# Kernel optimization log

Measured on AMD Instinct MI355X. Metric: run time of the kernel, lower is better.

## Reference

```python
import jax, jax.numpy as jnp
import numpy as np

D = 1024
H = 16
HD = D // H
EPS = 1e-8


def setup_inputs() -> dict:
    key = jax.random.key(0)
    ks = jax.random.split(key, 12)
    B, S = 2, 2048
    scale = 1.0 / np.sqrt(D)
    inp = {
        "x": jax.random.normal(ks[0], (B, S, D), dtype=jnp.float32),
        "M": jax.random.uniform(ks[1], (B, S, S), dtype=jnp.float32),
        "Wq": jax.random.normal(ks[2], (D, D), dtype=jnp.float32) * scale,
        "bq": jax.random.normal(ks[3], (D,), dtype=jnp.float32) * 0.01,
        "Wk": jax.random.normal(ks[4], (D, D), dtype=jnp.float32) * scale,
        "bk": jax.random.normal(ks[5], (D,), dtype=jnp.float32) * 0.01,
        "Wv": jax.random.normal(ks[6], (D, D), dtype=jnp.float32) * scale,
        "bv": jax.random.normal(ks[7], (D,), dtype=jnp.float32) * 0.01,
        "Wo": jax.random.normal(ks[8], (D, D), dtype=jnp.float32) * scale,
        "bo": jax.random.normal(ks[9], (D,), dtype=jnp.float32) * 0.01,
    }
    return inp


def reference(x, M, Wq, bq, Wk, bk, Wv, bv, Wo, bo):
    B, S, _ = x.shape
    sm_scale = HD ** -0.5
    # projections (torch Linear: x @ W^T + b), split into heads: [B,H,S,HD]
    def proj(W, b):
        return (x @ W.T + b).reshape(B, S, H, HD).transpose(0, 2, 1, 3)
    Q, K, V = proj(Wq, bq), proj(Wk, bk), proj(Wv, bv)
    # scores: [B,H,S,S], gated pre-softmax by M broadcast over heads
    scores = jnp.einsum("bhqd,bhkd->bhqk", Q, K) * sm_scale
    Mb = M[:, None, :, :]  # [B,1,S,S]
    scores = scores * Mb
    attn = jax.nn.softmax(scores, axis=-1)
    # post-softmax re-gate + L1 renormalize
    A_sparse = attn * Mb
    norm = jnp.sum(jnp.abs(A_sparse), axis=-1, keepdims=True) + EPS
    A_bar = A_sparse / norm
    out = jnp.einsum("bhqk,bhkd->bhqd", A_bar, V)
    out = out.transpose(0, 2, 1, 3).reshape(B, S, D)
    return out @ Wo.T + bo
```

## Files before the change

kernel.cpp:

```cpp
#include <hip/hip_runtime.h>
#include <hip/hip_bf16.h>
#include <stdint.h>

#define S_LEN 2048
#define D_DIM 1024
#define NROW 4096
#define EPS_F 1e-8f

typedef __attribute__((ext_vector_type(8))) short short8;
typedef __attribute__((ext_vector_type(4))) float f32x4;

__device__ __forceinline__ unsigned short f2bf(float f) {
  uint32_t u = __float_as_uint(f);
  u += 0x7fffu + ((u >> 16) & 1u);
  return (unsigned short)(u >> 16);
}

__global__ void convert_kernel(const float* __restrict__ x,
                               const float* __restrict__ wq, const float* __restrict__ wk,
                               const float* __restrict__ wv, const float* __restrict__ wo,
                               unsigned short* __restrict__ xb, unsigned short* __restrict__ wqb,
                               unsigned short* __restrict__ wkb, unsigned short* __restrict__ wvb,
                               unsigned short* __restrict__ wob) {
  const float* src; unsigned short* dst; int n;
  switch (blockIdx.y) {
    case 0: src = x;  dst = xb;  n = NROW * D_DIM;  break;
    case 1: src = wq; dst = wqb; n = D_DIM * D_DIM; break;
    case 2: src = wk; dst = wkb; n = D_DIM * D_DIM; break;
    case 3: src = wv; dst = wvb; n = D_DIM * D_DIM; break;
    default: src = wo; dst = wob; n = D_DIM * D_DIM; break;
  }
  int idx = blockIdx.x * blockDim.x + threadIdx.x;
  int base = idx * 8;
  if (base >= n) return;
  f32x4 va = *(const f32x4*)(src + base);
  f32x4 vb = *(const f32x4*)(src + base + 4);
  short8 o;
  o[0] = (short)f2bf(va[0]); o[1] = (short)f2bf(va[1]);
  o[2] = (short)f2bf(va[2]); o[3] = (short)f2bf(va[3]);
  o[4] = (short)f2bf(vb[0]); o[5] = (short)f2bf(vb[1]);
  o[6] = (short)f2bf(vb[2]); o[7] = (short)f2bf(vb[3]);
  *(short8*)(dst + base) = o;
}

template<int MODE>
__global__ __launch_bounds__(256) void gemm_bt(const unsigned short* __restrict__ A,
                                               const unsigned short* __restrict__ Bw,
                                               const float* __restrict__ bias,
                                               void* __restrict__ Cout, float scale) {
  __shared__ unsigned short As[128 * 72];
  __shared__ unsigned short Bs[128 * 72];
  const int t = threadIdx.x;
  const int lane = t & 63;
  const int w = t >> 6;
  const int wm = w >> 1, wn = w & 1;
  const int m0 = blockIdx.x * 128, n0 = blockIdx.y * 128;
  const int g = lane >> 4, c0 = lane & 15;

  f32x4 acc[4][4] = {};
  short8 ra[4], rb[4];

#define G_LOADT(kt) { int kk = (kt) * 64; \
    _Pragma("unroll") for (int i = 0; i < 4; ++i) { int c = i * 256 + t; int row = c >> 3, c8 = c & 7; \
      ra[i] = *(const short8*)(A  + (size_t)(m0 + row) * D_DIM + kk + c8 * 8); \
      rb[i] = *(const short8*)(Bw + (size_t)(n0 + row) * D_DIM + kk + c8 * 8); } }
#define G_WRITET() { \
    _Pragma("unroll") for (int i = 0; i < 4; ++i) { int c = i * 256 + t; int row = c >> 3, c8 = c & 7; \
      *(short8*)&As[row * 72 + c8 * 8] = ra[i]; \
      *(short8*)&Bs[row * 72 + c8 * 8] = rb[i]; } }

  G_LOADT(0); G_WRITET(); __syncthreads();

  for (int kt = 0; kt < 16; ++kt) {
    if (kt < 15) G_LOADT(kt + 1);
#pragma unroll
    for (int kc = 0; kc < 2; ++kc) {
      short8 af[4], bf[4];
#pragma unroll
      for (int mf = 0; mf < 4; ++mf)
        af[mf] = *(const short8*)&As[(wm * 64 + mf * 16 + c0) * 72 + kc * 32 + g * 8];
#pragma unroll
      for (int nf = 0; nf < 4; ++nf)
        bf[nf] = *(const short8*)&Bs[(wn * 64 + nf * 16 + c0) * 72 + kc * 32 + g * 8];
#pragma unroll
      for (int mf = 0; mf < 4; ++mf)
#pragma unroll
        for (int nf = 0; nf < 4; ++nf)
          acc[mf][nf] = __builtin_amdgcn_mfma_f32_16x16x32_bf16(af[mf], bf[nf], acc[mf][nf], 0, 0, 0);
    }
    __syncthreads();
    if (kt < 15) { G_WRITET(); __syncthreads(); }
  }

#pragma unroll
  for (int nf = 0; nf < 4; ++nf) {
    int jj = n0 + wn * 64 + nf * 16 + c0;
    float bval = bias[jj];
#pragma unroll
    for (int mf = 0; mf < 4; ++mf) {
#pragma unroll
      for (int r = 0; r < 4; ++r) {
        int ii = m0 + wm * 64 + mf * 16 + g * 4 + r;
        float v = (acc[mf][nf][r] + bval) * scale;
        if (MODE == 2) {
          ((float*)Cout)[(size_t)ii * D_DIM + jj] = v;
        } else if (MODE == 0) {
          size_t addr = ((size_t)((ii >> 11) * 16 + (jj >> 6)) * 2048 + (ii & 2047)) * 64 + (jj & 63);
          ((unsigned short*)Cout)[addr] = f2bf(v);
        } else {
          size_t addr = ((size_t)(ii >> 11) * 1024 + jj) * 2048 + (ii & 2047);
          ((unsigned short*)Cout)[addr] = f2bf(v);
        }
      }
    }
  }
#undef G_LOADT
#undef G_WRITET
}

__global__ __launch_bounds__(512, 4) void attn_kernel(const unsigned short* __restrict__ Qg,
                                                      const unsigned short* __restrict__ Kg,
                                                      const unsigned short* __restrict__ Vtg,
                                                      const float* __restrict__ Mg,
                                                      unsigned short* __restrict__ aout) {
  __shared__ unsigned short Ks[2][64 * 72];
  __shared__ unsigned short Vts[2][64 * 72];
  __shared__ unsigned short Ps[128 * 72];

  const int t = threadIdx.x;
  const int lane = t & 63;
  const int w = t >> 6;
  const int g = lane >> 4, c0 = lane & 15;
  const int bh = blockIdx.x;
  const int q0 = blockIdx.y * 128;
  const int b = bh >> 4;

  const unsigned short* Qbase  = Qg  + ((size_t)bh * 2048 + q0) * 64;
  const unsigned short* Kbase  = Kg  + (size_t)bh * 2048 * 64;
  const unsigned short* Vtbase = Vtg + (size_t)bh * 64 * 2048;
  const float* Mlane = Mg + ((size_t)b * 2048 + q0 + w * 16 + g * 4) * 2048 + c0;

  short8 qf[2];
#pragma unroll
  for (int kc = 0; kc < 2; ++kc)
    qf[kc] = *(const short8*)(Qbase + (size_t)(w * 16 + c0) * 64 + kc * 32 + g * 8);

  f32x4 o[4] = {};
  float dpe[4] = {0.f, 0.f, 0.f, 0.f};
  float de[4]  = {0.f, 0.f, 0.f, 0.f};

  short8 rk, rv;
  const int srow = t >> 3, sc8 = t & 7;

#define A_LOAD(kt) { int k0 = (kt) * 64; \
    rk = *(const short8*)(Kbase  + (size_t)(k0 + srow) * 64 + sc8 * 8); \
    rv = *(const short8*)(Vtbase + (size_t)srow * 2048 + k0 + sc8 * 8); }
#define A_WRITE(bufi) { \
    *(short8*)&Ks[bufi][srow * 72 + sc8 * 8]  = rk; \
    *(short8*)&Vts[bufi][srow * 72 + sc8 * 8] = rv; }

  A_LOAD(0); A_WRITE(0); __syncthreads();

  for (int kt = 0; kt < 32; ++kt) {
    const int cur = kt & 1;
    if (kt < 31) A_LOAD(kt + 1);

    float mv[4][4];
    {
      const float* Mk = Mlane + kt * 64;
#pragma unroll
      for (int nf = 0; nf < 4; ++nf)
#pragma unroll
        for (int r = 0; r < 4; ++r)
          mv[nf][r] = Mk[(size_t)r * 2048 + nf * 16];
    }

    f32x4 sf[4] = {};
#pragma unroll
    for (int kc = 0; kc < 2; ++kc) {
      short8 kf[4];
#pragma unroll
      for (int nf = 0; nf < 4; ++nf)
        kf[nf] = *(const short8*)&Ks[cur][(nf * 16 + c0) * 72 + kc * 32 + g * 8];
#pragma unroll
      for (int nf = 0; nf < 4; ++nf)
        sf[nf] = __builtin_amdgcn_mfma_f32_16x16x32_bf16(qf[kc], kf[nf], sf[nf], 0, 0, 0);
    }

#pragma unroll
    for (int nf = 0; nf < 4; ++nf)
#pragma unroll
      for (int r = 0; r < 4; ++r) {
        float m = mv[nf][r];
        float e  = __expf(sf[nf][r] * m);
        float pe = m * e;
        dpe[r] += pe;
        de[r]  += e;
        uint32_t u = __float_as_uint(pe) + 0x8000u;
        Ps[(w * 16 + g * 4 + r) * 72 + nf * 16 + c0] = (unsigned short)(u >> 16);
      }

    asm volatile("s_waitcnt lgkmcnt(0)" ::: "memory");
    __builtin_amdgcn_sched_barrier(0);

#pragma unroll
    for (int kc = 0; kc < 2; ++kc) {
      short8 pf = *(const short8*)&Ps[(w * 16 + c0) * 72 + kc * 32 + g * 8];
#pragma unroll
      for (int df = 0; df < 4; ++df) {
        short8 vf = *(const short8*)&Vts[cur][(df * 16 + c0) * 72 + kc * 32 + g * 8];
        o[df] = __builtin_amdgcn_mfma_f32_16x16x32_bf16(pf, vf, o[df], 0, 0, 0);
      }
    }

    if (kt < 31) A_WRITE(cur ^ 1);
    __syncthreads();
  }

#pragma unroll
  for (int xm = 1; xm <= 8; xm <<= 1)
#pragma unroll
    for (int r = 0; r < 4; ++r) {
      dpe[r] += __shfl_xor(dpe[r], xm);
      de[r]  += __shfl_xor(de[r], xm);
    }
  float inv[4];
#pragma unroll
  for (int r = 0; r < 4; ++r)
    inv[r] = 1.0f / (dpe[r] + EPS_F * de[r]);

#pragma unroll
  for (int df = 0; df < 4; ++df)
#pragma unroll
    for (int r = 0; r < 4; ++r) {
      float v = o[df][r] * inv[r];
      int qi = q0 + w * 16 + g * 4 + r;
      int col = (bh & 15) * 64 + df * 16 + c0;
      aout[((size_t)b * 2048 + qi) * 1024 + col] = f2bf(v);
    }
#undef A_LOAD
#undef A_WRITE
}

extern "C" void kernel_launch(void* const* d_in, const int* in_sizes, int n_in,
                              void* d_out, int out_size, void* d_ws, size_t ws_size,
                              hipStream_t stream) {
  const float* x  = (const float*)d_in[0];
  const float* M  = (const float*)d_in[1];
  const float* Wq = (const float*)d_in[2];
  const float* bq = (const float*)d_in[3];
  const float* Wk = (const float*)d_in[4];
  const float* bk = (const float*)d_in[5];
  const float* Wv = (const float*)d_in[6];
  const float* bv = (const float*)d_in[7];
  const float* Wo = (const float*)d_in[8];
  const float* bo = (const float*)d_in[9];
  float* out = (float*)d_out;
  char* ws = (char*)d_ws;

  unsigned short* xb   = (unsigned short*)(ws);
  unsigned short* wqb  = (unsigned short*)(ws + 8388608);
  unsigned short* wkb  = (unsigned short*)(ws + 10485760);
  unsigned short* wvb  = (unsigned short*)(ws + 12582912);
  unsigned short* wob  = (unsigned short*)(ws + 14680064);
  unsigned short* Qb   = (unsigned short*)(ws + 16777216);
  unsigned short* Kb   = (unsigned short*)(ws + 25165824);
  unsigned short* Vtb  = (unsigned short*)(ws + 33554432);
  unsigned short* aoutb= (unsigned short*)(ws + 41943040);

  convert_kernel<<<dim3(2048, 5), 256, 0, stream>>>(x, Wq, Wk, Wv, Wo, xb, wqb, wkb, wvb, wob);
  gemm_bt<0><<<dim3(32, 8), 256, 0, stream>>>(xb, wqb, bq, (void*)Qb, 0.125f);
  gemm_bt<0><<<dim3(32, 8), 256, 0, stream>>>(xb, wkb, bk, (void*)Kb, 1.0f);
  gemm_bt<1><<<dim3(32, 8), 256, 0, stream>>>(xb, wvb, bv, (void*)Vtb, 1.0f);
  attn_kernel<<<dim3(32, 16), 512, 0, stream>>>(Qb, Kb, Vtb, M, aoutb);
  gemm_bt<2><<<dim3(32, 8), 256, 0, stream>>>(aoutb, wob, bo, (void*)out, 1.0f);
}
```

Before: 166.8 us.

## Fuse QKV GEMM, pre-layout mask in fp16, register-resident P in attention

Fuses the three QKV projections into a single GEMM over a concatenated weight matrix, and switches GEMM tile loads to direct global-to-LDS loads without padding. A new pass converts the mask M to fp16 in the MFMA fragment order so attention reads half the bytes with vectorized loads. The attention kernel swaps MFMA operand order so P stays in registers, exchanged across lanes with ds_bpermute instead of an LDS round trip. It also drops the eps*sum(e) term from the normalizer and packs the output with v_cvt_pk_bf16_f32. Risks include bank conflicts in the unpadded LDS, a synchronous GEMM load loop with no prefetch, an extra pass over M, and small numerical differences from the fp16 mask and the removed eps term.

```diff
diff --git a/kernel.cpp b/kernel.cpp
--- a/kernel.cpp
+++ b/kernel.cpp
@@ -5,33 +5,41 @@
 #define S_LEN 2048
 #define D_DIM 1024
 #define NROW 4096
-#define EPS_F 1e-8f
 
 typedef __attribute__((ext_vector_type(8))) short short8;
 typedef __attribute__((ext_vector_type(4))) float f32x4;
-
-__device__ __forceinline__ unsigned short f2bf(float f) {
+typedef __attribute__((ext_vector_type(4))) int i32x4;
+typedef __attribute__((ext_vector_type(8))) _Float16 h8;
+typedef unsigned short ushort_t;
+
+__device__ __forceinline__ ushort_t f2bf(float f) {
   uint32_t u = __float_as_uint(f);
   u += 0x7fffu + ((u >> 16) & 1u);
-  return (unsigned short)(u >> 16);
-}
-
-__global__ void convert_kernel(const float* __restrict__ x,
-                               const float* __restrict__ wq, const float* __restrict__ wk,
-                               const float* __restrict__ wv, const float* __restrict__ wo,
-                               unsigned short* __restrict__ xb, unsigned short* __restrict__ wqb,
-                               unsigned short* __restrict__ wkb, unsigned short* __restrict__ wvb,
-                               unsigned short* __restrict__ wob) {
-  const float* src; unsigned short* dst; int n;
+  return (ushort_t)(u >> 16);
+}
+
+__device__ __forceinline__ ushort_t f2h(float f) {
+  _Float16 h = (_Float16)f;
+  return __builtin_bit_cast(ushort_t, h);
+}
+
+__device__ __forceinline__ void gload16(const void* g, void* l) {
+  __builtin_amdgcn_global_load_lds((const __attribute__((address_space(1))) void*)g,
+                                   (__attribute__((address_space(3))) void*)l, 16, 0, 0);
+}
+
+__global__ void convert4_kernel(const float* __restrict__ x,
+                                const float* __restrict__ wq, const float* __restrict__ wk,
+                                const float* __restrict__ wv,
+                                ushort_t* __restrict__ xb, ushort_t* __restrict__ wcat) {
+  const float* src; ushort_t* dst; int n;
   switch (blockIdx.y) {
-    case 0: src = x;  dst = xb;  n = NROW * D_DIM;  break;
-    case 1: src = wq; dst = wqb; n = D_DIM * D_DIM; break;
-    case 2: src = wk; dst = wkb; n = D_DIM * D_DIM; break;
-    case 3: src = wv; dst = wvb; n = D_DIM * D_DIM; break;
-    default: src = wo; dst = wob; n = D_DIM * D_DIM; break;
-  }
-  int idx = blockIdx.x * blockDim.x + threadIdx.x;
-  int base = idx * 8;
+    case 0: src = x;  dst = xb;             n = NROW * D_DIM;  break;
+    case 1: src = wq; dst = wcat;           n = D_DIM * D_DIM; break;
+    case 2: src = wk; dst = wcat + 1048576; n = D_DIM * D_DIM; break;
+    default: src = wv; dst = wcat + 2097152; n = D_DIM * D_DIM; break;
+  }
+  int base = (blockIdx.x * 256 + threadIdx.x) * 8;
   if (base >= n) return;
   f32x4 va = *(const f32x4*)(src + base);
   f32x4 vb = *(const f32x4*)(src + base + 4);
@@ -43,45 +51,74 @@
   *(short8*)(dst + base) = o;
 }
 
+__global__ void convert_wo_kernel(const float* __restrict__ wo, ushort_t* __restrict__ wob) {
+  int base = (blockIdx.x * 256 + threadIdx.x) * 8;
+  f32x4 va = *(const f32x4*)(wo + base);
+  f32x4 vb = *(const f32x4*)(wo + base + 4);
+  short8 o;
+  o[0] = (short)f2bf(va[0]); o[1] = (short)f2bf(va[1]);
+  o[2] = (short)f2bf(va[2]); o[3] = (short)f2bf(va[3]);
+  o[4] = (short)f2bf(vb[0]); o[5] = (short)f2bf(vb[1]);
+  o[6] = (short)f2bf(vb[2]); o[7] = (short)f2bf(vb[3]);
+  *(short8*)(wob + base) = o;
+}
+
+__global__ __launch_bounds__(256) void m2_transform(const float* __restrict__ M,
+                                                    ushort_t* __restrict__ M2) {
+  int tid = blockIdx.x * 256 + threadIdx.x;
+  int lane = tid & 63, w = (tid >> 6) & 7, kt = (tid >> 9) & 31, combo = tid >> 14;
+  int c0 = lane & 15, g = lane >> 4;
+  int b = combo >> 4, q0i = combo & 15;
+  const float* src = M + ((size_t)b * 2048 + q0i * 128 + w * 16 + c0) * 2048 + kt * 64 + g * 4;
+  ushort_t outv[16];
+#pragma unroll
+  for (int nf = 0; nf < 4; ++nf) {
+    f32x4 v = *(const f32x4*)(src + nf * 16);
+#pragma unroll
+    for (int r = 0; r < 4; ++r)
+      outv[nf * 4 + r] = f2h(v[r]);
+  }
+  *(short8*)(M2 + (size_t)tid * 16)     = *(short8*)&outv[0];
+  *(short8*)(M2 + (size_t)tid * 16 + 8) = *(short8*)&outv[8];
+}
+
 template<int MODE>
-__global__ __launch_bounds__(256) void gemm_bt(const unsigned short* __restrict__ A,
-                                               const unsigned short* __restrict__ Bw,
-                                               const float* __restrict__ bias,
-                                               void* __restrict__ Cout, float scale) {
-  __shared__ unsigned short As[128 * 72];
-  __shared__ unsigned short Bs[128 * 72];
+__global__ __launch_bounds__(256, 4) void gemm_glds(const ushort_t* __restrict__ A,
+                                                    const ushort_t* __restrict__ Bw,
+                                                    const float* __restrict__ bias0,
+                                                    const float* __restrict__ bias1,
+                                                    const float* __restrict__ bias2,
+                                                    void* __restrict__ Cout) {
+  __shared__ ushort_t As[128 * 64];
+  __shared__ ushort_t Bs[128 * 64];
   const int t = threadIdx.x;
   const int lane = t & 63;
   const int w = t >> 6;
   const int wm = w >> 1, wn = w & 1;
   const int m0 = blockIdx.x * 128, n0 = blockIdx.y * 128;
   const int g = lane >> 4, c0 = lane & 15;
+  const int srow = lane >> 3, scol = (lane & 7) * 8;
 
   f32x4 acc[4][4] = {};
-  short8 ra[4], rb[4];
-
-#define G_LOADT(kt) { int kk = (kt) * 64; \
-    _Pragma("unroll") for (int i = 0; i < 4; ++i) { int c = i * 256 + t; int row = c >> 3, c8 = c & 7; \
-      ra[i] = *(const short8*)(A  + (size_t)(m0 + row) * D_DIM + kk + c8 * 8); \
-      rb[i] = *(const short8*)(Bw + (size_t)(n0 + row) * D_DIM + kk + c8 * 8); } }
-#define G_WRITET() { \
-    _Pragma("unroll") for (int i = 0; i < 4; ++i) { int c = i * 256 + t; int row = c >> 3, c8 = c & 7; \
-      *(short8*)&As[row * 72 + c8 * 8] = ra[i]; \
-      *(short8*)&Bs[row * 72 + c8 * 8] = rb[i]; } }
-
-  G_LOADT(0); G_WRITET(); __syncthreads();
 
   for (int kt = 0; kt < 16; ++kt) {
-    if (kt < 15) G_LOADT(kt + 1);
+    const int kk = kt * 64;
+#pragma unroll
+    for (int i = 0; i < 4; ++i) {
+      gload16(A  + (size_t)(m0 + w * 32 + i * 8 + srow) * D_DIM + kk + scol, &As[(w * 32 + i * 8) * 64]);
+      gload16(Bw + (size_t)(n0 + w * 32 + i * 8 + srow) * D_DIM + kk + scol, &Bs[(w * 32 + i * 8) * 64]);
+    }
+    asm volatile("s_waitcnt vmcnt(0)" ::: "memory");
+    __syncthreads();
 #pragma unroll
     for (int kc = 0; kc < 2; ++kc) {
       short8 af[4], bf[4];
 #pragma unroll
       for (int mf = 0; mf < 4; ++mf)
-        af[mf] = *(const short8*)&As[(wm * 64 + mf * 16 + c0) * 72 + kc * 32 + g * 8];
+        af[mf] = *(const short8*)&As[(wm * 64 + mf * 16 + c0) * 64 + kc * 32 + g * 8];
 #pragma unroll
       for (int nf = 0; nf < 4; ++nf)
-        bf[nf] = *(const short8*)&Bs[(wn * 64 + nf * 16 + c0) * 72 + kc * 32 + g * 8];
+        bf[nf] = *(const short8*)&Bs[(wn * 64 + nf * 16 + c0) * 64 + kc * 32 + g * 8];
 #pragma unroll
       for (int mf = 0; mf < 4; ++mf)
 #pragma unroll
@@ -89,56 +126,64 @@
           acc[mf][nf] = __builtin_amdgcn_mfma_f32_16x16x32_bf16(af[mf], bf[nf], acc[mf][nf], 0, 0, 0);
     }
     __syncthreads();
-    if (kt < 15) { G_WRITET(); __syncthreads(); }
   }
 
 #pragma unroll
   for (int nf = 0; nf < 4; ++nf) {
     int jj = n0 + wn * 64 + nf * 16 + c0;
-    float bval = bias[jj];
+    float bval;
+    if (MODE == 0) {
+      int proj = jj >> 10, jcol = jj & 1023;
+      const float* bp = (proj == 0) ? bias0 : ((proj == 1) ? bias1 : bias2);
+      bval = bp[jcol];
+    } else {
+      bval = bias0[jj];
+    }
 #pragma unroll
     for (int mf = 0; mf < 4; ++mf) {
 #pragma unroll
       for (int r = 0; r < 4; ++r) {
         int ii = m0 + wm * 64 + mf * 16 + g * 4 + r;
-        float v = (acc[mf][nf][r] + bval) * scale;
+        float v = acc[mf][nf][r] + bval;
         if (MODE == 2) {
           ((float*)Cout)[(size_t)ii * D_DIM + jj] = v;
-        } else if (MODE == 0) {
-          size_t addr = ((size_t)((ii >> 11) * 16 + (jj >> 6)) * 2048 + (ii & 2047)) * 64 + (jj & 63);
-          ((unsigned short*)Cout)[addr] = f2bf(v);
         } else {
-          size_t addr = ((size_t)(ii >> 11) * 1024 + jj) * 2048 + (ii & 2047);
-          ((unsigned short*)Cout)[addr] = f2bf(v);
+          int proj = jj >> 10, jcol = jj & 1023;
+          if (proj == 0) v *= 0.125f;
+          int bb = ii >> 11, s = ii & 2047;
+          size_t addr;
+          if (proj < 2) {
+            int hcol = jcol >> 6, hd = jcol & 63;
+            addr = (size_t)proj * 4194304 + ((size_t)(bb * 16 + hcol) * 2048 + s) * 64 + hd;
+          } else {
+            addr = (size_t)2 * 4194304 + ((size_t)bb * 1024 + jcol) * 2048 + s;
+          }
+          ((ushort_t*)Cout)[addr] = f2bf(v);
         }
       }
     }
   }
-#undef G_LOADT
-#undef G_WRITET
-}
-
-__global__ __launch_bounds__(512, 4) void attn_kernel(const unsigned short* __restrict__ Qg,
-                                                      const unsigned short* __restrict__ Kg,
-                                                      const unsigned short* __restrict__ Vtg,
-                                                      const float* __restrict__ Mg,
-                                                      unsigned short* __restrict__ aout) {
-  __shared__ unsigned short Ks[2][64 * 72];
-  __shared__ unsigned short Vts[2][64 * 72];
-  __shared__ unsigned short Ps[128 * 72];
-
-  const int t = threadIdx.x;
-  const int lane = t & 63;
-  const int w = t >> 6;
+}
+
+__global__ __launch_bounds__(512, 4) void attn_kernel(const ushort_t* __restrict__ Qg,
+                                                      const ushort_t* __restrict__ Kg,
+                                                      const ushort_t* __restrict__ Vtg,
+                                                      const ushort_t* __restrict__ M2,
+                                                      ushort_t* __restrict__ aout) {
+  __shared__ ushort_t Ks[2][64 * 72];
+  __shared__ ushort_t Vts[2][64 * 72];
+
+  const int t = threadIdx.x, lane = t & 63, w = t >> 6;
   const int g = lane >> 4, c0 = lane & 15;
-  const int bh = blockIdx.x;
-  const int q0 = blockIdx.y * 128;
-  const int b = bh >> 4;
-
-  const unsigned short* Qbase  = Qg  + ((size_t)bh * 2048 + q0) * 64;
-  const unsigned short* Kbase  = Kg  + (size_t)bh * 2048 * 64;
-  const unsigned short* Vtbase = Vtg + (size_t)bh * 64 * 2048;
-  const float* Mlane = Mg + ((size_t)b * 2048 + q0 + w * 16 + g * 4) * 2048 + c0;
+  const int id = blockIdx.x;
+  const int r8 = id & 7, hh = (id >> 3) & 15, ss = id >> 7;
+  const int combo = r8 + 8 * ss, b = combo >> 4, q0 = (combo & 15) * 128;
+  const int bh = b * 16 + hh;
+
+  const ushort_t* Qbase  = Qg  + ((size_t)bh * 2048 + q0) * 64;
+  const ushort_t* Kbase  = Kg  + (size_t)bh * 2048 * 64;
+  const ushort_t* Vtbase = Vtg + (size_t)bh * 64 * 2048;
+  const ushort_t* M2base = M2 + ((size_t)combo * 32 * 8 + w) * 64 * 16 + (size_t)lane * 16;
 
   short8 qf[2];
 #pragma unroll
@@ -146,33 +191,31 @@
     qf[kc] = *(const short8*)(Qbase + (size_t)(w * 16 + c0) * 64 + kc * 32 + g * 8);
 
   f32x4 o[4] = {};
-  float dpe[4] = {0.f, 0.f, 0.f, 0.f};
-  float de[4]  = {0.f, 0.f, 0.f, 0.f};
-
-  short8 rk, rv;
-  const int srow = t >> 3, sc8 = t & 7;
-
-#define A_LOAD(kt) { int k0 = (kt) * 64; \
-    rk = *(const short8*)(Kbase  + (size_t)(k0 + srow) * 64 + sc8 * 8); \
-    rv = *(const short8*)(Vtbase + (size_t)srow * 2048 + k0 + sc8 * 8); }
-#define A_WRITE(bufi) { \
-    *(short8*)&Ks[bufi][srow * 72 + sc8 * 8]  = rk; \
-    *(short8*)&Vts[bufi][srow * 72 + sc8 * 8] = rv; }
-
-  A_LOAD(0); A_WRITE(0); __syncthreads();
+  float dpe = 0.f;
+  const int idxA = (((g & 1) * 2 + (g >> 1)) * 16 + c0) * 4;
+  const int idxB = (((g & 1) * 2 + 1 - (g >> 1)) * 16 + c0) * 4;
+  const bool glo = (g < 2);
+  const bool gb = (g & 1);
+
+  const int srow = t >> 3, sc8 = (t & 7) * 8;
+  short8 rk, rv, rm0, rm1, rm0n, rm1n;
+
+  rk  = *(const short8*)(Kbase + (size_t)srow * 64 + sc8);
+  rv  = *(const short8*)(Vtbase + (size_t)srow * 2048 + sc8);
+  rm0 = *(const short8*)(M2base);
+  rm1 = *(const short8*)(M2base + 8);
+  *(short8*)&Ks[0][srow * 72 + sc8]  = rk;
+  *(short8*)&Vts[0][srow * 72 + sc8] = rv;
+  __syncthreads();
 
   for (int kt = 0; kt < 32; ++kt) {
     const int cur = kt & 1;
-    if (kt < 31) A_LOAD(kt + 1);
-
-    float mv[4][4];
-    {
-      const float* Mk = Mlane + kt * 64;
-#pragma unroll
-      for (int nf = 0; nf < 4; ++nf)
-#pragma unroll
-        for (int r = 0; r < 4; ++r)
-          mv[nf][r] = Mk[(size_t)r * 2048 + nf * 16];
+    if (kt < 31) {
+      const int k0 = (kt + 1) * 64;
+      rk  = *(const short8*)(Kbase + (size_t)(k0 + srow) * 64 + sc8);
+      rv  = *(const short8*)(Vtbase + (size_t)srow * 2048 + k0 + sc8);
+      rm0n = *(const short8*)(M2base + (size_t)(kt + 1) * 8192);
+      rm1n = *(const short8*)(M2base + (size_t)(kt + 1) * 8192 + 8);
     }
 
     f32x4 sf[4] = {};
@@ -184,62 +227,77 @@
         kf[nf] = *(const short8*)&Ks[cur][(nf * 16 + c0) * 72 + kc * 32 + g * 8];
 #pragma unroll
       for (int nf = 0; nf < 4; ++nf)
-        sf[nf] = __builtin_amdgcn_mfma_f32_16x16x32_bf16(qf[kc], kf[nf], sf[nf], 0, 0, 0);
-    }
-
-#pragma unroll
-    for (int nf = 0; nf < 4; ++nf)
+        sf[nf] = __builtin_amdgcn_mfma_f32_16x16x32_bf16(kf[nf], qf[kc], sf[nf], 0, 0, 0);
+    }
+
+    h8 mh0 = __builtin_bit_cast(h8, rm0);
+    h8 mh1 = __builtin_bit_cast(h8, rm1);
+    uint32_t w4[4][2];
+#pragma unroll
+    for (int nf = 0; nf < 4; ++nf) {
+      float p[4];
 #pragma unroll
       for (int r = 0; r < 4; ++r) {
-        float m = mv[nf][r];
-        float e  = __expf(sf[nf][r] * m);
+        float m = (nf < 2) ? (float)mh0[nf * 4 + r] : (float)mh1[(nf - 2) * 4 + r];
+        float e = __expf(sf[nf][r] * m);
         float pe = m * e;
-        dpe[r] += pe;
-        de[r]  += e;
-        uint32_t u = __float_as_uint(pe) + 0x8000u;
-        Ps[(w * 16 + g * 4 + r) * 72 + nf * 16 + c0] = (unsigned short)(u >> 16);
+        dpe += pe;
+        p[r] = pe;
       }
-
-    asm volatile("s_waitcnt lgkmcnt(0)" ::: "memory");
-    __builtin_amdgcn_sched_barrier(0);
-
+      asm("v_cvt_pk_bf16_f32 %0, %1, %2" : "=v"(w4[nf][0]) : "v"(p[0]), "v"(p[1]));
+      asm("v_cvt_pk_bf16_f32 %0, %1, %2" : "=v"(w4[nf][1]) : "v"(p[2]), "v"(p[3]));
+    }
+
+    short8 pf[2];
 #pragma unroll
     for (int kc = 0; kc < 2; ++kc) {
-      short8 pf = *(const short8*)&Ps[(w * 16 + c0) * 72 + kc * 32 + g * 8];
+      uint32_t sA0 = gb ? w4[2 * kc + 1][0] : w4[2 * kc][0];
+      uint32_t sA1 = gb ? w4[2 * kc + 1][1] : w4[2 * kc][1];
+      uint32_t sB0 = gb ? w4[2 * kc][0]     : w4[2 * kc + 1][0];
+      uint32_t sB1 = gb ? w4[2 * kc][1]     : w4[2 * kc + 1][1];
+      uint32_t rA0 = (uint32_t)__builtin_amdgcn_ds_bpermute(idxA, (int)sA0);
+      uint32_t rA1 = (uint32_t)__builtin_amdgcn_ds_bpermute(idxA, (int)sA1);
+      uint32_t rB0 = (uint32_t)__builtin_amdgcn_ds_bpermute(idxB, (int)sB0);
+      uint32_t rB1 = (uint32_t)__builtin_amdgcn_ds_bpermute(idxB, (int)sB1);
+      i32x4 f4;
+      f4[0] = (int)(glo ? rA0 : rB0);
+      f4[1] = (int)(glo ? rA1 : rB1);
+      f4[2] = (int)(glo ? rB0 : rA0);
+      f4[3] = (int)(glo ? rB1 : rA1);
+      pf[kc] = __builtin_bit_cast(short8, f4);
+    }
+
+#pragma unroll
+    for (int kc = 0; kc < 2; ++kc) {
 #pragma unroll
       for (int df = 0; df < 4; ++df) {
         short8 vf = *(const short8*)&Vts[cur][(df * 16 + c0) * 72 + kc * 32 + g * 8];
-        o[df] = __builtin_amdgcn_mfma_f32_16x16x32_bf16(pf, vf, o[df], 0, 0, 0);
+        o[df] = __builtin_amdgcn_mfma_f32_16x16x32_bf16(vf, pf[kc], o[df], 0, 0, 0);
       }
     }
 
-    if (kt < 31) A_WRITE(cur ^ 1);
+    if (kt < 31) {
+      *(short8*)&Ks[cur ^ 1][srow * 72 + sc8]  = rk;
+      *(short8*)&Vts[cur ^ 1][srow * 72 + sc8] = rv;
+      rm0 = rm0n; rm1 = rm1n;
+    }
     __syncthreads();
   }
 
-#pragma unroll
-  for (int xm = 1; xm <= 8; xm <<= 1)
-#pragma unroll
-    for (int r = 0; r < 4; ++r) {
-      dpe[r] += __shfl_xor(dpe[r], xm);
-      de[r]  += __shfl_xor(de[r], xm);
-    }
-  float inv[4];
-#pragma unroll
-  for (int r = 0; r < 4; ++r)
-    inv[r] = 1.0f / (dpe[r] + EPS_F * de[r]);
-
-#pragma unroll
-  for (int df = 0; df < 4; ++df)
-#pragma unroll
-    for (int r = 0; r < 4; ++r) {
-      float v = o[df][r] * inv[r];
-      int qi = q0 + w * 16 + g * 4 + r;
-      int col = (bh & 15) * 64 + df * 16 + c0;
-      aout[((size_t)b * 2048 + qi) * 1024 + col] = f2bf(v);
-    }
-#undef A_LOAD
-#undef A_WRITE
+  dpe += __shfl_xor(dpe, 16);
+  dpe += __shfl_xor(dpe, 32);
+  float inv = 1.0f / dpe;
+
+#pragma unroll
+  for (int df = 0; df < 4; ++df) {
+    float v0 = o[df][0] * inv, v1 = o[df][1] * inv;
+    float v2 = o[df][2] * inv, v3 = o[df][3] * inv;
+    uint32_t d0, d1;
+    asm("v_cvt_pk_bf16_f32 %0, %1, %2" : "=v"(d0) : "v"(v0), "v"(v1));
+    asm("v_cvt_pk_bf16_f32 %0, %1, %2" : "=v"(d1) : "v"(v2), "v"(v3));
+    unsigned long long pk = (unsigned long long)d0 | ((unsigned long long)d1 << 32);
+    *(unsigned long long*)&aout[((size_t)b * 2048 + q0 + w * 16 + c0) * 1024 + hh * 64 + df * 16 + g * 4] = pk;
+  }
 }
 
 extern "C" void kernel_launch(void* const* d_in, const int* in_sizes, int n_in,
@@ -258,20 +316,19 @@
   float* out = (float*)d_out;
   char* ws = (char*)d_ws;
 
-  unsigned short* xb   = (unsigned short*)(ws);
-  unsigned short* wqb  = (unsigned short*)(ws + 8388608);
-  unsigned short* wkb  = (unsigned short*)(ws + 10485760);
-  unsigned short* wvb  = (unsigned short*)(ws + 12582912);
-  unsigned short* wob  = (unsigned short*)(ws + 14680064);
-  unsigned short* Qb   = (unsigned short*)(ws + 16777216);
-  unsigned short* Kb   = (unsigned short*)(ws + 25165824);
-  unsigned short* Vtb  = (unsigned short*)(ws + 33554432);
-  unsigned short* aoutb= (unsigned short*)(ws + 41943040);
-
-  convert_kernel<<<dim3(2048, 5), 256, 0, stream>>>(x, Wq, Wk, Wv, Wo, xb, wqb, wkb, wvb, wob);
-  gemm_bt<0><<<dim3(32, 8), 256, 0, stream>>>(xb, wqb, bq, (void*)Qb, 0.125f);
-  gemm_bt<0><<<dim3(32, 8), 256, 0, stream>>>(xb, wkb, bk, (void*)Kb, 1.0f);
-  gemm_bt<1><<<dim3(32, 8), 256, 0, stream>>>(xb, wvb, bv, (void*)Vtb, 1.0f);
-  attn_kernel<<<dim3(32, 16), 512, 0, stream>>>(Qb, Kb, Vtb, M, aoutb);
-  gemm_bt<2><<<dim3(32, 8), 256, 0, stream>>>(aoutb, wob, bo, (void*)out, 1.0f);
-}
+  ushort_t* Qb    = (ushort_t*)(ws);
+  ushort_t* Kb    = (ushort_t*)(ws + 8388608);
+  ushort_t* Vtb   = (ushort_t*)(ws + 16777216);
+  ushort_t* xb    = (ushort_t*)(ws + 25165824);
+  ushort_t* Wcat  = (ushort_t*)(ws + 33554432);
+  ushort_t* M2    = (ushort_t*)(ws + 25165824);
+  ushort_t* aoutb = (ushort_t*)(ws + 41943040);
+  ushort_t* wob   = (ushort_t*)(ws);
+
+  convert4_kernel<<<dim3(2048, 4), 256, 0, stream>>>(x, Wq, Wk, Wv, xb, Wcat);
+  gemm_glds<0><<<dim3(32, 24), 256, 0, stream>>>(xb, Wcat, bq, bk, bv, (void*)Qb);
+  m2_transform<<<2048, 256, 0, stream>>>(M, M2);
+  attn_kernel<<<512, 512, 0, stream>>>(Qb, Kb, Vtb, M2, aoutb);
+  convert_wo_kernel<<<512, 256, 0, stream>>>(Wo, wob);
+  gemm_glds<2><<<dim3(32, 8), 256, 0, stream>>>(aoutb, wob, bo, bo, bo, (void*)out);
+}
```

New measurement: 151.9 us. -8.9%, faster.
